# Kernel tuning notes

Hardware: AMD Instinct MI355X
Metric: run time of the kernel (lower is better)

Reference implementation:

```python
import jax, jax.numpy as jnp
import numpy as np

T, H = 2048, 1024          # tokens, hidden_size
NH, NKV, D = 16, 4, 64     # heads, kv heads, head_dim
E, F = 8, 1024             # experts, intermediate_size
TOPK = 1
EPS = 1e-5
THETA = 500000.0
SCALE = D ** -0.5


def rmsnorm(x, w=None, eps=EPS):
    # fp32 accumulation like vLLM RMSNorm
    v = jnp.mean(x.astype(jnp.float32) ** 2, axis=-1, keepdims=True)
    y = x.astype(jnp.float32) * jax.lax.rsqrt(v + eps)
    y = y.astype(x.dtype)
    return y * w if w is not None else y


def setup_inputs() -> dict:
    key = jax.random.key(0)
    ks = jax.random.split(key, 12)
    s = 1.0 / np.sqrt(H)
    sf = 1.0 / np.sqrt(F)
    return {
        "positions": jnp.arange(T, dtype=jnp.int32),
        "hidden_states": jax.random.normal(ks[0], (T, H), jnp.float32),
        "ln1_w": jnp.ones((H,), jnp.float32),
        "ln2_w": jnp.ones((H,), jnp.float32),
        "wqkv": jax.random.normal(ks[1], (H, (NH + 2 * NKV) * D), jnp.float32) * s,
        "wo": jax.random.normal(ks[2], (NH * D, H), jnp.float32) * s,
        "router_w": jax.random.normal(ks[3], (H, E), jnp.float32) * s,
        "w_gate": jax.random.normal(ks[4], (E, H, F), jnp.float32) * s,
        "w_up": jax.random.normal(ks[5], (E, H, F), jnp.float32) * s,
        "w_down": jax.random.normal(ks[6], (E, F, H), jnp.float32) * sf,
        "sh_gate": jax.random.normal(ks[7], (H, F), jnp.float32) * s,
        "sh_up": jax.random.normal(ks[8], (H, F), jnp.float32) * s,
        "sh_down": jax.random.normal(ks[9], (F, H), jnp.float32) * sf,
    }


def reference(positions, hidden_states, ln1_w, ln2_w, wqkv, wo, router_w,
              w_gate, w_up, w_down, sh_gate, sh_up, sh_down):
    # --- input_layernorm (residual is None on first call) ---
    residual = hidden_states
    h = rmsnorm(hidden_states, ln1_w)

    # --- attention: qkv proj ---
    qkv = h @ wqkv
    q = qkv[:, : NH * D].reshape(T, NH, D)
    k = qkv[:, NH * D: (NH + NKV) * D].reshape(T, NKV, D)
    v = qkv[:, (NH + NKV) * D:].reshape(T, NKV, D)

    # --- neox-style RoPE ---
    half = D // 2
    inv_freq = 1.0 / (THETA ** (jnp.arange(half, dtype=jnp.float32) / half))
    ang = positions.astype(jnp.float32)[:, None] * inv_freq[None, :]
    cos = jnp.cos(ang)[:, None, :]  # [T,1,half]
    sin = jnp.sin(ang)[:, None, :]

    def rope(x):
        x1, x2 = x[..., :half], x[..., half:]
        return jnp.concatenate([x1 * cos - x2 * sin, x2 * cos + x1 * sin], axis=-1)

    q = rope(q)
    k = rope(k)

    # --- fp32 QK-RMSNorm (no weight), applied after RoPE as in source ---
    q = rmsnorm(q)
    k = rmsnorm(k)

    # --- GQA causal attention ---
    n_rep = NH // NKV
    kr = jnp.repeat(k, n_rep, axis=1)  # [T,NH,D]
    vr = jnp.repeat(v, n_rep, axis=1)
    scores = jnp.einsum('thd,shd->hts', q, kr) * SCALE  # [NH,T,T]
    causal = positions[:, None] >= positions[None, :]
    scores = jnp.where(causal[None], scores, -jnp.inf)
    attn = jax.nn.softmax(scores, axis=-1)
    ao = jnp.einsum('hts,shd->thd', attn, vr).reshape(T, NH * D)
    h = ao @ wo

    # --- post_attention_layernorm with fused residual add ---
    x = h + residual
    residual = x
    h = rmsnorm(x, ln2_w)

    # --- MoE: top-1 sigmoid router, router weight applied on input ---
    logits = h @ router_w                      # [T,E]
    score, idx = jax.lax.top_k(logits, TOPK)   # [T,1]
    gate = jax.nn.sigmoid(score.astype(jnp.float32)).astype(h.dtype)
    x_in = h * gate                            # apply_router_weight_on_input
    onehot = (idx == jnp.arange(E)[None, :]).astype(h.dtype)  # [T,E]
    g = jax.nn.silu(jnp.einsum('th,ehf->tef', x_in, w_gate)) \
        * jnp.einsum('th,ehf->tef', x_in, w_up)               # [T,E,F]
    out_e = jnp.einsum('tef,efh->teh', g, w_down)             # [T,E,H]
    routed = jnp.einsum('teh,te->th', out_e, onehot)

    # --- shared expert (SiLU MLP) ---
    shared = (jax.nn.silu(h @ sh_gate) * (h @ sh_up)) @ sh_down

    out = routed + shared
    return (out, residual)
```

## Files before the change

### kernel.cpp

```cpp
#include <hip/hip_runtime.h>
#include <hip/hip_bf16.h>
#include <cmath>
#include <cstdint>

#define T 2048
#define H 1024
#define NH 16
#define NKV 4
#define DH 64
#define NE 8
#define FF 1024
#define QKVN ((NH + 2 * NKV) * DH)
#define EPS 1e-5f
#define ATTN_SCALE 0.125f
#define LOG2E 1.44269504f
#define MBOUND 12.0f
#define ASPLIT 4

typedef short bf16x8 __attribute__((ext_vector_type(8)));
typedef float floatx4 __attribute__((ext_vector_type(4)));

__device__ __forceinline__ void gload16(const void* g, void* l) {
  __builtin_amdgcn_global_load_lds((const __attribute__((address_space(1))) void*)g,
                                   (__attribute__((address_space(3))) void*)l, 16, 0, 0);
}

__global__ __launch_bounds__(256) void rmsnorm1024(const float* __restrict__ x,
                                                   const float* __restrict__ w,
                                                   __hip_bfloat16* __restrict__ yb) {
  int row = blockIdx.x;
  const float4* x4 = (const float4*)(x + (size_t)row * H);
  float4 v = x4[threadIdx.x];
  float s = v.x * v.x + v.y * v.y + v.z * v.z + v.w * v.w;
  #pragma unroll
  for (int o = 32; o; o >>= 1) s += __shfl_down(s, o, 64);
  __shared__ float red[4];
  if ((threadIdx.x & 63) == 0) red[threadIdx.x >> 6] = s;
  __syncthreads();
  s = red[0] + red[1] + red[2] + red[3];
  float inv = rsqrtf(s * (1.0f / (float)H) + EPS);
  float4 wv = ((const float4*)w)[threadIdx.x];
  __hip_bfloat16* yp = yb + (size_t)row * H + threadIdx.x * 4;
  yp[0] = __float2bfloat16(v.x * inv * wv.x);
  yp[1] = __float2bfloat16(v.y * inv * wv.y);
  yp[2] = __float2bfloat16(v.z * inv * wv.z);
  yp[3] = __float2bfloat16(v.w * inv * wv.w);
}

__global__ __launch_bounds__(256) void fused_add_rms(const float* __restrict__ a,
                                                     const float* __restrict__ b,
                                                     float* __restrict__ resid,
                                                     const float* __restrict__ w,
                                                     float* __restrict__ yf,
                                                     __hip_bfloat16* __restrict__ yb,
                                                     int* __restrict__ counts_g) {
  int row = blockIdx.x;
  if (row == 0 && threadIdx.x < 2 * NE) counts_g[threadIdx.x] = 0;
  float4 av = ((const float4*)(a + (size_t)row * H))[threadIdx.x];
  float4 bv = ((const float4*)(b + (size_t)row * H))[threadIdx.x];
  float4 v = make_float4(av.x + bv.x, av.y + bv.y, av.z + bv.z, av.w + bv.w);
  ((float4*)(resid + (size_t)row * H))[threadIdx.x] = v;
  float s = v.x * v.x + v.y * v.y + v.z * v.z + v.w * v.w;
  #pragma unroll
  for (int o = 32; o; o >>= 1) s += __shfl_down(s, o, 64);
  __shared__ float red[4];
  if ((threadIdx.x & 63) == 0) red[threadIdx.x >> 6] = s;
  __syncthreads();
  s = red[0] + red[1] + red[2] + red[3];
  float inv = rsqrtf(s * (1.0f / (float)H) + EPS);
  float4 wv = ((const float4*)w)[threadIdx.x];
  float o0 = v.x * inv * wv.x, o1 = v.y * inv * wv.y, o2 = v.z * inv * wv.z, o3 = v.w * inv * wv.w;
  ((float4*)(yf + (size_t)row * H))[threadIdx.x] = make_float4(o0, o1, o2, o3);
  __hip_bfloat16* yp = yb + (size_t)row * H + threadIdx.x * 4;
  yp[0] = __float2bfloat16(o0);
  yp[1] = __float2bfloat16(o1);
  yp[2] = __float2bfloat16(o2);
  yp[3] = __float2bfloat16(o3);
}

__global__ __launch_bounds__(256) void tcast9(const float* __restrict__ srcE,
                                              const float* __restrict__ srcS,
                                              __hip_bfloat16* __restrict__ dst, int R, int C,
                                              long long srcStride, long long dstStride,
                                              long long sBatch, long long dBatch) {
  int z = blockIdx.z;
  const float* src = (srcS && z == (int)gridDim.z - 1) ? srcS : srcE + (long long)z * sBatch;
  dst += (long long)z * dBatch;
  int c0 = blockIdx.x * 64, r0 = blockIdx.y * 32;
  __shared__ float tile[32][65];
  int tid = threadIdx.x;
  int lr = tid >> 4;
  int lc = (tid & 15) * 4;
  #pragma unroll
  for (int it = 0; it < 2; it++) {
    float4 v = *(const float4*)(src + (long long)(r0 + lr + it * 16) * srcStride + c0 + lc);
    tile[lr + it * 16][lc + 0] = v.x;
    tile[lr + it * 16][lc + 1] = v.y;
    tile[lr + it * 16][lc + 2] = v.z;
    tile[lr + it * 16][lc + 3] = v.w;
  }
  __syncthreads();
  int oc = tid >> 2;
  int rr = (tid & 3) * 8;
  short ov[8];
  #pragma unroll
  for (int i = 0; i < 8; i++) {
    __hip_bfloat16 b = __float2bfloat16(tile[rr + i][oc]);
    ov[i] = *(short*)&b;
  }
  *(bf16x8*)((short*)dst + (long long)(c0 + oc) * dstStride + r0 + rr) = *(bf16x8*)ov;
}

__global__ __launch_bounds__(256) void gemm_bf16(const __hip_bfloat16* __restrict__ A,
                                                 const __hip_bfloat16* __restrict__ A2,
                                                 const __hip_bfloat16* __restrict__ Bt,
                                                 void* __restrict__ Cout, void* __restrict__ Cout2,
                                                 int M, int N, int K, int out_bf16,
                                                 const int* __restrict__ row_offs,
                                                 long long strideB,
                                                 const int* __restrict__ permA,
                                                 const float* __restrict__ gatev) {
  int e = blockIdx.z;
  bool sh = (A2 != nullptr && e == (int)gridDim.z - 1);
  int rbeg = 0, rend = M;
  const __hip_bfloat16* Ap = A;
  void* Cp = Cout;
  const int* pA = permA;
  if (sh) {
    Ap = A2; Cp = Cout2; pA = nullptr;
  } else if (row_offs) {
    rbeg = row_offs[e]; rend = row_offs[e + 1];
  }
  long long m0 = rbeg + (long long)blockIdx.y * 128;
  if (m0 >= rend) return;
  long long n0 = (long long)blockIdx.x * 64;
  const __hip_bfloat16* Bp = Bt + (long long)e * strideB;

  __shared__ unsigned short As[2][128 * 64];
  __shared__ unsigned short Bs[2][64 * 64];

  int tid = threadIdx.x;
  int lane = tid & 63, w = tid >> 6;
  int wr = (w >> 1) * 64, wc = (w & 1) * 32;
  int qd = lane >> 4, ln16 = lane & 15;
  int l7 = ln16 & 7;

  floatx4 acc[4][2];
  floatx4 zero = {0.f, 0.f, 0.f, 0.f};
  #pragma unroll
  for (int i = 0; i < 4; i++)
    #pragma unroll
    for (int j = 0; j < 2; j++) acc[i][j] = zero;

  int rowA[4], kcA[4];
  const unsigned short* Arow[4];
  const unsigned short* Brow[2];
  #pragma unroll
  for (int it = 0; it < 4; it++) {
    int chunk = tid + it * 256;
    rowA[it] = chunk >> 3;
    kcA[it] = ((chunk & 7) ^ (rowA[it] & 7)) * 8;
    long long ra = m0 + rowA[it];
    if (ra >= rend) ra = rend - 1;
    long long tok = pA ? (long long)pA[ra] : ra;
    Arow[it] = (const unsigned short*)Ap + tok * K;
  }
  #pragma unroll
  for (int it = 0; it < 2; it++)
    Brow[it] = (const unsigned short*)Bp + (n0 + rowA[it]) * K;

  #pragma unroll
  for (int it = 0; it < 4; it++)
    gload16(Arow[it] + kcA[it], As[0] + (tid + it * 256) * 8);
  #pragma unroll
  for (int it = 0; it < 2; it++)
    gload16(Brow[it] + kcA[it], Bs[0] + (tid + it * 256) * 8);
  __syncthreads();

  int cur = 0;
  for (int k0 = 0; k0 < K; k0 += 64) {
    int kn = k0 + 64;
    if (kn < K) {
      #pragma unroll
      for (int it = 0; it < 4; it++)
        gload16(Arow[it] + kn + kcA[it], As[cur ^ 1] + (tid + it * 256) * 8);
      #pragma unroll
      for (int it = 0; it < 2; it++)
        gload16(Brow[it] + kn + kcA[it], Bs[cur ^ 1] + (tid + it * 256) * 8);
    }
    const unsigned short* Ac = As[cur];
    const unsigned short* Bc = Bs[cur];
    #pragma unroll
    for (int s = 0; s < 2; s++) {
      bf16x8 af[4], bfr[2];
      #pragma unroll
      for (int i = 0; i < 4; i++) {
        int row = wr + i * 16 + ln16;
        af[i] = *(const bf16x8*)(Ac + row * 64 + (((s * 4 + qd) ^ l7) * 8));
      }
      #pragma unroll
      for (int j = 0; j < 2; j++) {
        int row = wc + j * 16 + ln16;
        bfr[j] = *(const bf16x8*)(Bc + row * 64 + (((s * 4 + qd) ^ l7) * 8));
      }
      #pragma unroll
      for (int i = 0; i < 4; i++)
        #pragma unroll
        for (int j = 0; j < 2; j++)
          acc[i][j] = __builtin_amdgcn_mfma_f32_16x16x32_bf16(af[i], bfr[j], acc[i][j], 0, 0, 0);
    }
    __syncthreads();
    cur ^= 1;
  }

  #pragma unroll
  for (int i = 0; i < 4; i++) {
    #pragma unroll
    for (int r = 0; r < 4; r++) {
      long long gm = m0 + wr + i * 16 + qd * 4 + r;
      if (gm < rend) {
        float gsc = 1.0f;
        if (pA && gatev) gsc = gatev[pA[gm]];
        #pragma unroll
        for (int j = 0; j < 2; j++) {
          long long gn = n0 + wc + j * 16 + ln16;
          float v = acc[i][j][r] * gsc;
          if (out_bf16)
            ((__hip_bfloat16*)Cp)[gm * N + gn] = __float2bfloat16(v);
          else
            ((float*)Cp)[gm * N + gn] = v;
        }
      }
    }
  }
}

__global__ __launch_bounds__(256) void rope_pack(const float* __restrict__ qkv,
                                                 const int* __restrict__ positions,
                                                 __hip_bfloat16* __restrict__ Qb,
                                                 __hip_bfloat16* __restrict__ Kb) {
  int b = blockIdx.x * 4 + (threadIdx.x >> 6);
  int t = b / (NH + NKV);
  int hh = b % (NH + NKV);
  const float* ptr = qkv + (long long)t * QKVN + hh * DH;
  int d = threadIdx.x & 63;
  float v = ptr[d];
  int fi = d & 31;
  float inv_freq = exp2f(-(float)fi * (18.93156857f / 32.0f));
  float ang = (float)positions[t] * inv_freq;
  float c = __cosf(ang), s = __sinf(ang);
  float other = __shfl_xor(v, 32, 64);
  float r = (d < 32) ? (v * c - other * s) : (v * c + other * s);
  float sq = r * r;
  #pragma unroll
  for (int off = 32; off; off >>= 1) sq += __shfl_xor(sq, off, 64);
  float o = r * rsqrtf(sq * (1.0f / (float)DH) + EPS);
  if (hh < NH)
    Qb[(size_t)t * (NH * DH) + hh * DH + d] = __float2bfloat16(o * (ATTN_SCALE * LOG2E));
  else
    Kb[(size_t)t * (NKV * DH) + (hh - NH) * DH + d] = __float2bfloat16(o);
}

__global__ __launch_bounds__(256, 2) void attn_mfma(const __hip_bfloat16* __restrict__ Qb,
                                                    const __hip_bfloat16* __restrict__ Kbuf,
                                                    const __hip_bfloat16* __restrict__ VtG,
                                                    float* __restrict__ Opart,
                                                    float* __restrict__ Lpart) {
  int kvh = blockIdx.y;
  int qi = blockIdx.x;
  int sp = blockIdx.z;
  int q0 = qi * 64;
  int nt = qi + 1;
  if (sp >= nt) return;

  __shared__ unsigned short Ks[2][64 * 64];
  __shared__ unsigned short Vs[2][64 * 64];
  __shared__ unsigned short Ps[4 * 16 * 64];

  int tid = threadIdx.x;
  int lane = tid & 63, w = tid >> 6;
  int h = kvh * 4 + w;
  int qd = lane >> 4, ln16 = lane & 15;
  int l7 = ln16 & 7;
  unsigned short* Pw = Ps + w * 16 * 64;

  int r0 = tid >> 3;
  int sc = ((tid & 7) ^ (r0 & 7)) * 8;

  const unsigned short* KbP = (const unsigned short*)Kbuf;
  const unsigned short* VtP = (const unsigned short*)VtG;

  bf16x8 aq[4][2];
  #pragma unroll
  for (int rt = 0; rt < 4; rt++) {
    const unsigned short* qp =
        (const unsigned short*)Qb + (size_t)(q0 + rt * 16 + ln16) * (NH * DH) + h * DH;
    aq[rt][0] = *(const bf16x8*)(qp + qd * 8);
    aq[rt][1] = *(const bf16x8*)(qp + 32 + qd * 8);
  }

  bf16x8 ones;
  #pragma unroll
  for (int i = 0; i < 8; i++) ones[i] = (short)0x3F80;

  floatx4 O_[4][4], accl[4];
  floatx4 zero = {0.f, 0.f, 0.f, 0.f};
  #pragma unroll
  for (int rt = 0; rt < 4; rt++) {
    #pragma unroll
    for (int j = 0; j < 4; j++) O_[rt][j] = zero;
    accl[rt] = zero;
  }

  {
    int kb = sp * 64;
    gload16(KbP + (size_t)(kb + r0) * (NKV * DH) + kvh * DH + sc, Ks[0] + tid * 8);
    gload16(KbP + (size_t)(kb + r0 + 32) * (NKV * DH) + kvh * DH + sc, Ks[0] + tid * 8 + 2048);
    gload16(VtP + (size_t)(kvh * DH + r0) * T + kb + sc, Vs[0] + tid * 8);
    gload16(VtP + (size_t)(kvh * DH + r0 + 32) * T + kb + sc, Vs[0] + tid * 8 + 2048);
  }
  __syncthreads();

  int cur = 0;
  for (int kt = sp; kt < nt; kt += ASPLIT) {
    int ktn = kt + ASPLIT;
    if (ktn < nt) {
      int kb = ktn * 64;
      unsigned short* Kn = Ks[cur ^ 1];
      unsigned short* Vn = Vs[cur ^ 1];
      gload16(KbP + (size_t)(kb + r0) * (NKV * DH) + kvh * DH + sc, Kn + tid * 8);
      gload16(KbP + (size_t)(kb + r0 + 32) * (NKV * DH) + kvh * DH + sc, Kn + tid * 8 + 2048);
      gload16(VtP + (size_t)(kvh * DH + r0) * T + kb + sc, Vn + tid * 8);
      gload16(VtP + (size_t)(kvh * DH + r0 + 32) * T + kb + sc, Vn + tid * 8 + 2048);
    }
    const unsigned short* Kc = Ks[cur];
    const unsigned short* Vc = Vs[cur];
    int kb = kt * 64;

    #pragma unroll
    for (int rt = 0; rt < 4; rt++) {
      floatx4 S_[4];
      #pragma unroll
      for (int j = 0; j < 4; j++) S_[j] = zero;
      #pragma unroll
      for (int s = 0; s < 2; s++) {
        bf16x8 bk[4];
        #pragma unroll
        for (int j = 0; j < 4; j++)
          bk[j] = *(const bf16x8*)(Kc + (j * 16 + ln16) * 64 + (((s * 4 + qd) ^ l7) * 8));
        #pragma unroll
        for (int j = 0; j < 4; j++)
          S_[j] = __builtin_amdgcn_mfma_f32_16x16x32_bf16(aq[rt][s], bk[j], S_[j], 0, 0, 0);
      }

      int tq_base = q0 + rt * 16 + qd * 4;
      if (kb + 63 > q0 + rt * 16) {
        #pragma unroll
        for (int j = 0; j < 4; j++) {
          int tk = kb + j * 16 + ln16;
          #pragma unroll
          for (int r = 0; r < 4; r++)
            S_[j][r] = (tk <= tq_base + r) ? exp2f(S_[j][r] - MBOUND) : 0.f;
        }
      } else {
        #pragma unroll
        for (int j = 0; j < 4; j++)
          #pragma unroll
          for (int r = 0; r < 4; r++) S_[j][r] = exp2f(S_[j][r] - MBOUND);
      }

      #pragma unroll
      for (int j = 0; j < 4; j++)
        #pragma unroll
        for (int r = 0; r < 4; r++) {
          int row = qd * 4 + r;
          int pc = (((j * 2 + (ln16 >> 3)) ^ (row & 7)) * 8) + l7;
          __hip_bfloat16 pb = __float2bfloat16(S_[j][r]);
          Pw[row * 64 + pc] = *(unsigned short*)&pb;
        }

      #pragma unroll
      for (int s = 0; s < 2; s++) {
        bf16x8 ap = *(const bf16x8*)(Pw + ln16 * 64 + (((s * 4 + qd) ^ l7) * 8));
        bf16x8 bv[4];
        #pragma unroll
        for (int j = 0; j < 4; j++)
          bv[j] = *(const bf16x8*)(Vc + (j * 16 + ln16) * 64 + (((s * 4 + qd) ^ l7) * 8));
        #pragma unroll
        for (int j = 0; j < 4; j++)
          O_[rt][j] = __builtin_amdgcn_mfma_f32_16x16x32_bf16(ap, bv[j], O_[rt][j], 0, 0, 0);
        accl[rt] = __builtin_amdgcn_mfma_f32_16x16x32_bf16(ap, ones, accl[rt], 0, 0, 0);
      }
    }
    __syncthreads();
    cur ^= 1;
  }

  size_t pbase = ((size_t)(qi * NH + h) * ASPLIT + sp) * (64 * 64);
  #pragma unroll
  for (int rt = 0; rt < 4; rt++) {
    int rl_base = rt * 16 + qd * 4;
    #pragma unroll
    for (int j = 0; j < 4; j++)
      #pragma unroll
      for (int r = 0; r < 4; r++)
        Opart[pbase + (size_t)(rl_base + r) * 64 + j * 16 + ln16] = O_[rt][j][r];
  }
  if (ln16 == 0) {
    size_t lbase = ((size_t)(qi * NH + h) * ASPLIT + sp) * 64;
    #pragma unroll
    for (int rt = 0; rt < 4; rt++)
      #pragma unroll
      for (int r = 0; r < 4; r++) Lpart[lbase + rt * 16 + qd * 4 + r] = accl[rt][r];
  }
}

__global__ __launch_bounds__(256) void attn_combine(const float* __restrict__ Opart,
                                                    const float* __restrict__ Lpart,
                                                    __hip_bfloat16* __restrict__ ao) {
  int qi = blockIdx.x, h = blockIdx.y;
  int nv = (qi + 1 < ASPLIT) ? (qi + 1) : ASPLIT;
  int row = threadIdx.x >> 2;
  int c0 = (threadIdx.x & 3) * 16;
  size_t base = (size_t)(qi * NH + h) * ASPLIT * 4096;
  size_t lb = (size_t)(qi * NH + h) * ASPLIT * 64;
  float l = 0.f;
  float acc[16];
  #pragma unroll
  for (int i = 0; i < 16; i++) acc[i] = 0.f;
  for (int s = 0; s < nv; s++) {
    const float* Op = Opart + base + (size_t)s * 4096 + (size_t)row * 64 + c0;
    l += Lpart[lb + s * 64 + row];
    #pragma unroll
    for (int i = 0; i < 16; i += 4) {
      float4 v = *(const float4*)(Op + i);
      acc[i] += v.x; acc[i + 1] += v.y; acc[i + 2] += v.z; acc[i + 3] += v.w;
    }
  }
  float inv = 1.f / l;
  int t = qi * 64 + row;
  short ov[16];
  #pragma unroll
  for (int i = 0; i < 16; i++) {
    __hip_bfloat16 b = __float2bfloat16(acc[i] * inv);
    ov[i] = *(short*)&b;
  }
  short* dst = (short*)ao + (size_t)t * (NH * DH) + h * DH + c0;
  *(bf16x8*)dst = *(bf16x8*)&ov[0];
  *(bf16x8*)(dst + 8) = *(bf16x8*)&ov[8];
}

__global__ __launch_bounds__(256) void silumul_both(const __hip_bfloat16* __restrict__ gA2,
                                                    const __hip_bfloat16* __restrict__ gS2,
                                                    __hip_bfloat16* __restrict__ gP,
                                                    __hip_bfloat16* __restrict__ gPs,
                                                    int n8each) {
  int i = blockIdx.x * blockDim.x + threadIdx.x;
  const __hip_bfloat16* src = gA2;
  __hip_bfloat16* dst = gP;
  if (i >= n8each) {
    i -= n8each;
    src = gS2;
    dst = gPs;
  }
  int el = i * 8;
  int row = el >> 10;
  int c = el & (FF - 1);
  const unsigned short* g = (const unsigned short*)src + (size_t)row * (2 * FF) + c;
  bf16x8 a8 = *(const bf16x8*)g;
  bf16x8 b8 = *(const bf16x8*)(g + FF);
  short o8[8];
  #pragma unroll
  for (int k = 0; k < 8; k++) {
    short sa = a8[k], sb = b8[k];
    float av = __bfloat162float(*(__hip_bfloat16*)&sa);
    float bv = __bfloat162float(*(__hip_bfloat16*)&sb);
    __hip_bfloat16 ob = __float2bfloat16(av / (1.f + __expf(-av)) * bv);
    o8[k] = *(short*)&ob;
  }
  *(bf16x8*)((unsigned short*)dst + el) = *(bf16x8*)o8;
}

__global__ __launch_bounds__(64) void router_kernel(const float* __restrict__ h2,
                                                    const float* __restrict__ rw,
                                                    int* __restrict__ idx,
                                                    float* __restrict__ gate,
                                                    int* __restrict__ counts) {
  int t = blockIdx.x;
  int lane = threadIdx.x;
  float acc[NE] = {};
  for (int k = lane; k < H; k += 64) {
    float hv = h2[(long long)t * H + k];
    float4 r0 = *(const float4*)(rw + (long long)k * NE);
    float4 r1 = *(const float4*)(rw + (long long)k * NE + 4);
    acc[0] += hv * r0.x; acc[1] += hv * r0.y; acc[2] += hv * r0.z; acc[3] += hv * r0.w;
    acc[4] += hv * r1.x; acc[5] += hv * r1.y; acc[6] += hv * r1.z; acc[7] += hv * r1.w;
  }
  #pragma unroll
  for (int off = 32; off; off >>= 1)
    #pragma unroll
    for (int e2 = 0; e2 < NE; e2++) acc[e2] += __shfl_down(acc[e2], off, 64);
  if (lane == 0) {
    int best = 0;
    float bv = acc[0];
    #pragma unroll
    for (int e2 = 1; e2 < NE; e2++)
      if (acc[e2] > bv) { bv = acc[e2]; best = e2; }
    idx[t] = best;
    gate[t] = 1.f / (1.f + expf(-bv));
    atomicAdd(&counts[best], 1);
  }
}

__global__ __launch_bounds__(256) void assign_scan(const int* __restrict__ counts,
                                                   const int* __restrict__ idx,
                                                   int* __restrict__ offs,
                                                   int* __restrict__ cnt2,
                                                   int* __restrict__ perm,
                                                   int* __restrict__ pos) {
  __shared__ int offs_s[NE + 1];
  if (threadIdx.x == 0) {
    int s = 0;
    for (int e2 = 0; e2 < NE; e2++) { offs_s[e2] = s; offs[e2] = s; s += counts[e2]; }
    offs_s[NE] = s; offs[NE] = s;
  }
  __syncthreads();
  for (int t = threadIdx.x; t < T; t += 256) {
    int e2 = idx[t];
    int p = offs_s[e2] + atomicAdd(&cnt2[e2], 1);
    pos[t] = p;
    perm[p] = t;
  }
}

__global__ __launch_bounds__(256) void final_add_kernel(float* __restrict__ out,
                                                        const float* __restrict__ outp,
                                                        const int* __restrict__ pos) {
  int t = blockIdx.x;
  int p = pos[t];
  const float4* src = (const float4*)(outp + (long long)p * H);
  float4* dst = (float4*)(out + (long long)t * H);
  float4 a = dst[threadIdx.x];
  float4 b = src[threadIdx.x];
  a.x += b.x; a.y += b.y; a.z += b.z; a.w += b.w;
  dst[threadIdx.x] = a;
}

extern "C" void kernel_launch(void* const* d_in, const int* in_sizes, int n_in,
                              void* d_out, int out_size, void* d_ws, size_t ws_size,
                              hipStream_t stream) {
  const int* positions = (const int*)d_in[0];
  const float* hidden = (const float*)d_in[1];
  const float* ln1_w = (const float*)d_in[2];
  const float* ln2_w = (const float*)d_in[3];
  const float* wqkv = (const float*)d_in[4];
  const float* wo = (const float*)d_in[5];
  const float* router_w = (const float*)d_in[6];
  const float* w_gate = (const float*)d_in[7];
  const float* w_up = (const float*)d_in[8];
  const float* w_down = (const float*)d_in[9];
  const float* sh_gate = (const float*)d_in[10];
  const float* sh_up = (const float*)d_in[11];
  const float* sh_down = (const float*)d_in[12];

  float* out = (float*)d_out;
  float* resid = out + (size_t)T * H;

  char* p = (char*)d_ws;
  auto alloc = [&](size_t bytes) { char* r = p; p += (bytes + 255) & ~(size_t)255; return r; };

  float* qkv = (float*)alloc((size_t)T * QKVN * 4);
  float* h2 = (float*)alloc((size_t)T * H * 4);
  float* gb1 = (float*)alloc((size_t)T * H * 4);
  float* outp = (float*)alloc((size_t)T * H * 4);
  __hip_bfloat16* h1b = (__hip_bfloat16*)alloc((size_t)T * H * 2);
  __hip_bfloat16* aob = (__hip_bfloat16*)alloc((size_t)T * H * 2);
  __hip_bfloat16* h2b = (__hip_bfloat16*)alloc((size_t)T * H * 2);
  __hip_bfloat16* gA2 = (__hip_bfloat16*)alloc((size_t)T * 2 * FF * 2);
  __hip_bfloat16* gP = (__hip_bfloat16*)alloc((size_t)T * FF * 2);
  __hip_bfloat16* Qb = (__hip_bfloat16*)alloc((size_t)T * NH * DH * 2);
  __hip_bfloat16* Kb = (__hip_bfloat16*)alloc((size_t)T * NKV * DH * 2);
  __hip_bfloat16* VtG = (__hip_bfloat16*)alloc((size_t)NKV * DH * T * 2);
  __hip_bfloat16* wqkvT = (__hip_bfloat16*)alloc((size_t)H * QKVN * 2);
  __hip_bfloat16* woT = (__hip_bfloat16*)alloc((size_t)H * H * 2);
  __hip_bfloat16* wguT = (__hip_bfloat16*)alloc((size_t)9 * 2 * FF * H * 2);
  __hip_bfloat16* wdT = (__hip_bfloat16*)alloc((size_t)9 * H * FF * 2);
  int* counts = (int*)alloc(2 * NE * 4);
  int* cnt2 = counts + NE;
  int* offs = (int*)alloc((NE + 1) * 4);
  int* idx = (int*)alloc(T * 4);
  int* perm = (int*)alloc(T * 4);
  int* pos = (int*)alloc(T * 4);
  float* gate = (float*)alloc(T * 4);

  __hip_bfloat16* gS2 = (__hip_bfloat16*)gb1;
  __hip_bfloat16* gPs = h1b;

  float* Opart = qkv;
  float* Lpart = qkv + (size_t)(T / 64) * NH * ASPLIT * 4096;

  tcast9<<<dim3(QKVN / 64, H / 32, 1), 256, 0, stream>>>(wqkv, nullptr, wqkvT, H, QKVN, QKVN, H, 0, 0);
  tcast9<<<dim3(H / 64, H / 32, 1), 256, 0, stream>>>(wo, nullptr, woT, H, H, H, H, 0, 0);
  tcast9<<<dim3(FF / 64, H / 32, 9), 256, 0, stream>>>(w_gate, sh_gate, wguT, H, FF, FF, H,
                                                       (long long)H * FF, (long long)2 * H * FF);
  tcast9<<<dim3(FF / 64, H / 32, 9), 256, 0, stream>>>(w_up, sh_up, wguT + (size_t)FF * H, H, FF, FF, H,
                                                       (long long)H * FF, (long long)2 * H * FF);
  tcast9<<<dim3(H / 64, FF / 32, 9), 256, 0, stream>>>(w_down, sh_down, wdT, FF, H, H, FF,
                                                       (long long)FF * H, (long long)H * FF);

  rmsnorm1024<<<T, 256, 0, stream>>>(hidden, ln1_w, h1b);
  gemm_bf16<<<dim3(QKVN / 64, T / 128, 1), 256, 0, stream>>>(h1b, nullptr, wqkvT, qkv, nullptr,
                                                             T, QKVN, H, 0, nullptr, 0, nullptr, nullptr);
  rope_pack<<<T * (NH + NKV) / 4, 256, 0, stream>>>(qkv, positions, Qb, Kb);
  tcast9<<<dim3(NKV * DH / 64, T / 32, 1), 256, 0, stream>>>(qkv + (NH + NKV) * DH, nullptr, VtG,
                                                             T, NKV * DH, QKVN, T, 0, 0);
  attn_mfma<<<dim3(T / 64, NKV, ASPLIT), 256, 0, stream>>>(Qb, Kb, VtG, Opart, Lpart);
  attn_combine<<<dim3(T / 64, NH), 256, 0, stream>>>(Opart, Lpart, aob);
  gemm_bf16<<<dim3(H / 64, T / 128, 1), 256, 0, stream>>>(aob, nullptr, woT, gb1, nullptr,
                                                          T, H, H, 0, nullptr, 0, nullptr, nullptr);
  fused_add_rms<<<T, 256, 0, stream>>>(gb1, hidden, resid, ln2_w, h2, h2b, counts);
  router_kernel<<<T, 64, 0, stream>>>(h2, router_w, idx, gate, counts);
  assign_scan<<<1, 256, 0, stream>>>(counts, idx, offs, cnt2, perm, pos);
  gemm_bf16<<<dim3(2 * FF / 64, T / 128, 9), 256, 0, stream>>>(h2b, h2b, wguT, gA2, gS2,
                                                               T, 2 * FF, H, 1, offs,
                                                               (long long)2 * H * FF, perm, gate);
  silumul_both<<<(2 * T * FF / 8) / 256, 256, 0, stream>>>(gA2, gS2, gP, gPs, T * FF / 8);
  gemm_bf16<<<dim3(H / 64, T / 128, 9), 256, 0, stream>>>(gP, gPs, wdT, outp, out,
                                                          T, H, FF, 0, offs, (long long)FF * H,
                                                          nullptr, nullptr);
  final_add_kernel<<<T, 256, 0, stream>>>(out, outp, pos);
}
```

Baseline: 394.9 us.

## Fuse RoPE/QK-norm/V-transpose into QKV GEMM epilogue and residual add into O-proj

Adds a dedicated QKV GEMM whose 64-wide column tiles align with heads, so the epilogue applies RoPE, per-head RMS normalisation and scaling directly and writes bf16 Q/K, or transposes V through LDS into VtG. This removes the fp32 qkv round trip plus the separate rope_pack and transpose launches. The output-projection GEMM now adds the residual in its epilogue, reducing fused_add_rms to a plain RMS norm. The trade-off is a heavier GEMM epilogue with per-element sincos and more register pressure.

```diff
diff --git a/kernel.cpp b/kernel.cpp
--- a/kernel.cpp
+++ b/kernel.cpp
@@ -47,19 +47,14 @@
   yp[3] = __float2bfloat16(v.w * inv * wv.w);
 }
 
-__global__ __launch_bounds__(256) void fused_add_rms(const float* __restrict__ a,
-                                                     const float* __restrict__ b,
-                                                     float* __restrict__ resid,
-                                                     const float* __restrict__ w,
-                                                     float* __restrict__ yf,
-                                                     __hip_bfloat16* __restrict__ yb,
-                                                     int* __restrict__ counts_g) {
+__global__ __launch_bounds__(256) void rms_h2(const float* __restrict__ x,
+                                              const float* __restrict__ w,
+                                              float* __restrict__ yf,
+                                              __hip_bfloat16* __restrict__ yb,
+                                              int* __restrict__ counts_g) {
   int row = blockIdx.x;
   if (row == 0 && threadIdx.x < 2 * NE) counts_g[threadIdx.x] = 0;
-  float4 av = ((const float4*)(a + (size_t)row * H))[threadIdx.x];
-  float4 bv = ((const float4*)(b + (size_t)row * H))[threadIdx.x];
-  float4 v = make_float4(av.x + bv.x, av.y + bv.y, av.z + bv.z, av.w + bv.w);
-  ((float4*)(resid + (size_t)row * H))[threadIdx.x] = v;
+  float4 v = ((const float4*)(x + (size_t)row * H))[threadIdx.x];
   float s = v.x * v.x + v.y * v.y + v.z * v.z + v.w * v.w;
   #pragma unroll
   for (int o = 32; o; o >>= 1) s += __shfl_down(s, o, 64);
@@ -119,7 +114,8 @@
                                                  const int* __restrict__ row_offs,
                                                  long long strideB,
                                                  const int* __restrict__ permA,
-                                                 const float* __restrict__ gatev) {
+                                                 const float* __restrict__ gatev,
+                                                 const float* __restrict__ addC) {
   int e = blockIdx.z;
   bool sh = (A2 != nullptr && e == (int)gridDim.z - 1);
   int rbeg = 0, rend = M;
@@ -225,6 +221,7 @@
         for (int j = 0; j < 2; j++) {
           long long gn = n0 + wc + j * 16 + ln16;
           float v = acc[i][j][r] * gsc;
+          if (addC) v += addC[gm * N + gn];
           if (out_bf16)
             ((__hip_bfloat16*)Cp)[gm * N + gn] = __float2bfloat16(v);
           else
@@ -235,30 +232,146 @@
   }
 }
 
-__global__ __launch_bounds__(256) void rope_pack(const float* __restrict__ qkv,
-                                                 const int* __restrict__ positions,
-                                                 __hip_bfloat16* __restrict__ Qb,
-                                                 __hip_bfloat16* __restrict__ Kb) {
-  int b = blockIdx.x * 4 + (threadIdx.x >> 6);
-  int t = b / (NH + NKV);
-  int hh = b % (NH + NKV);
-  const float* ptr = qkv + (long long)t * QKVN + hh * DH;
-  int d = threadIdx.x & 63;
-  float v = ptr[d];
-  int fi = d & 31;
-  float inv_freq = exp2f(-(float)fi * (18.93156857f / 32.0f));
-  float ang = (float)positions[t] * inv_freq;
-  float c = __cosf(ang), s = __sinf(ang);
-  float other = __shfl_xor(v, 32, 64);
-  float r = (d < 32) ? (v * c - other * s) : (v * c + other * s);
-  float sq = r * r;
-  #pragma unroll
-  for (int off = 32; off; off >>= 1) sq += __shfl_xor(sq, off, 64);
-  float o = r * rsqrtf(sq * (1.0f / (float)DH) + EPS);
-  if (hh < NH)
-    Qb[(size_t)t * (NH * DH) + hh * DH + d] = __float2bfloat16(o * (ATTN_SCALE * LOG2E));
-  else
-    Kb[(size_t)t * (NKV * DH) + (hh - NH) * DH + d] = __float2bfloat16(o);
+__global__ __launch_bounds__(256) void gemm_qkv(const __hip_bfloat16* __restrict__ A,
+                                                const __hip_bfloat16* __restrict__ Bt,
+                                                const int* __restrict__ positions,
+                                                __hip_bfloat16* __restrict__ Qb,
+                                                __hip_bfloat16* __restrict__ Kb,
+                                                __hip_bfloat16* __restrict__ VtG) {
+  const int K = H;
+  long long m0 = (long long)blockIdx.y * 128;
+  long long n0 = (long long)blockIdx.x * 64;
+
+  __shared__ unsigned short As[2][128 * 64];
+  __shared__ unsigned short Bs[2][64 * 64];
+
+  int tid = threadIdx.x;
+  int lane = tid & 63, w = tid >> 6;
+  int qd = lane >> 4, ln16 = lane & 15;
+  int l7 = ln16 & 7;
+
+  floatx4 acc[2][4];
+  floatx4 zero = {0.f, 0.f, 0.f, 0.f};
+  #pragma unroll
+  for (int i = 0; i < 2; i++)
+    #pragma unroll
+    for (int j = 0; j < 4; j++) acc[i][j] = zero;
+
+  int rowA[4], kcA[4];
+  const unsigned short* Arow[4];
+  const unsigned short* Brow[2];
+  #pragma unroll
+  for (int it = 0; it < 4; it++) {
+    int chunk = tid + it * 256;
+    rowA[it] = chunk >> 3;
+    kcA[it] = ((chunk & 7) ^ (rowA[it] & 7)) * 8;
+    Arow[it] = (const unsigned short*)A + (m0 + rowA[it]) * K;
+  }
+  #pragma unroll
+  for (int it = 0; it < 2; it++)
+    Brow[it] = (const unsigned short*)Bt + (n0 + rowA[it]) * K;
+
+  #pragma unroll
+  for (int it = 0; it < 4; it++)
+    gload16(Arow[it] + kcA[it], As[0] + (tid + it * 256) * 8);
+  #pragma unroll
+  for (int it = 0; it < 2; it++)
+    gload16(Brow[it] + kcA[it], Bs[0] + (tid + it * 256) * 8);
+  __syncthreads();
+
+  int cur = 0;
+  for (int k0 = 0; k0 < K; k0 += 64) {
+    int kn = k0 + 64;
+    if (kn < K) {
+      #pragma unroll
+      for (int it = 0; it < 4; it++)
+        gload16(Arow[it] + kn + kcA[it], As[cur ^ 1] + (tid + it * 256) * 8);
+      #pragma unroll
+      for (int it = 0; it < 2; it++)
+        gload16(Brow[it] + kn + kcA[it], Bs[cur ^ 1] + (tid + it * 256) * 8);
+    }
+    const unsigned short* Ac = As[cur];
+    const unsigned short* Bc = Bs[cur];
+    #pragma unroll
+    for (int s = 0; s < 2; s++) {
+      bf16x8 af[2], bfr[4];
+      #pragma unroll
+      for (int i = 0; i < 2; i++) {
+        int row = w * 32 + i * 16 + ln16;
+        af[i] = *(const bf16x8*)(Ac + row * 64 + (((s * 4 + qd) ^ l7) * 8));
+      }
+      #pragma unroll
+      for (int j = 0; j < 4; j++) {
+        int row = j * 16 + ln16;
+        bfr[j] = *(const bf16x8*)(Bc + row * 64 + (((s * 4 + qd) ^ l7) * 8));
+      }
+      #pragma unroll
+      for (int i = 0; i < 2; i++)
+        #pragma unroll
+        for (int j = 0; j < 4; j++)
+          acc[i][j] = __builtin_amdgcn_mfma_f32_16x16x32_bf16(af[i], bfr[j], acc[i][j], 0, 0, 0);
+    }
+    __syncthreads();
+    cur ^= 1;
+  }
+
+  int hh = blockIdx.x;
+  if (hh < NH + NKV) {
+    bool isq = hh < NH;
+    float invf0 = exp2f(-(float)ln16 * (18.93156857f / 32.0f));
+    float invf1 = exp2f(-(float)(ln16 + 16) * (18.93156857f / 32.0f));
+    #pragma unroll
+    for (int i = 0; i < 2; i++) {
+      #pragma unroll
+      for (int r = 0; r < 4; r++) {
+        int t = (int)m0 + w * 32 + i * 16 + qd * 4 + r;
+        float pos = (float)positions[t];
+        float c0, s0, c1, s1;
+        __sincosf(pos * invf0, &s0, &c0);
+        __sincosf(pos * invf1, &s1, &c1);
+        float v0 = acc[i][0][r], v1 = acc[i][1][r], v2 = acc[i][2][r], v3 = acc[i][3][r];
+        float ro0 = v0 * c0 - v2 * s0;
+        float ro1 = v1 * c1 - v3 * s1;
+        float ro2 = v2 * c0 + v0 * s0;
+        float ro3 = v3 * c1 + v1 * s1;
+        float sq = ro0 * ro0 + ro1 * ro1 + ro2 * ro2 + ro3 * ro3;
+        sq += __shfl_xor(sq, 1, 64);
+        sq += __shfl_xor(sq, 2, 64);
+        sq += __shfl_xor(sq, 4, 64);
+        sq += __shfl_xor(sq, 8, 64);
+        float inv = rsqrtf(sq * (1.0f / (float)DH) + EPS);
+        if (isq) inv *= (ATTN_SCALE * LOG2E);
+        __hip_bfloat16* dst = isq ? (Qb + (size_t)t * (NH * DH) + hh * DH)
+                                  : (Kb + (size_t)t * (NKV * DH) + (hh - NH) * DH);
+        dst[0 * 16 + ln16] = __float2bfloat16(ro0 * inv);
+        dst[1 * 16 + ln16] = __float2bfloat16(ro1 * inv);
+        dst[2 * 16 + ln16] = __float2bfloat16(ro2 * inv);
+        dst[3 * 16 + ln16] = __float2bfloat16(ro3 * inv);
+      }
+    }
+  } else {
+    unsigned short* sw = ((unsigned short*)As) + w * 2560;
+    #pragma unroll
+    for (int i = 0; i < 2; i++)
+      #pragma unroll
+      for (int j = 0; j < 4; j++)
+        #pragma unroll
+        for (int r = 0; r < 4; r++) {
+          __hip_bfloat16 b = __float2bfloat16(acc[i][j][r]);
+          sw[(j * 16 + ln16) * 40 + i * 16 + qd * 4 + r] = *(unsigned short*)&b;
+        }
+    int d = lane;
+    int t0 = (int)m0 + w * 32;
+    const unsigned short* sr = sw + d * 40;
+    unsigned short* vd = (unsigned short*)VtG + (size_t)((hh - NH - NKV) * DH + d) * T + t0;
+    #pragma unroll
+    for (int kk = 0; kk < 4; kk++) {
+      short tmp[8];
+      #pragma unroll
+      for (int q2 = 0; q2 < 8; q2++) tmp[q2] = sr[kk * 8 + q2];
+      *(bf16x8*)(vd + kk * 8) = *(bf16x8*)tmp;
+    }
+  }
 }
 
 __global__ __launch_bounds__(256, 2) void attn_mfma(const __hip_bfloat16* __restrict__ Qb,
@@ -609,24 +722,22 @@
                                                        (long long)FF * H, (long long)H * FF);
 
   rmsnorm1024<<<T, 256, 0, stream>>>(hidden, ln1_w, h1b);
-  gemm_bf16<<<dim3(QKVN / 64, T / 128, 1), 256, 0, stream>>>(h1b, nullptr, wqkvT, qkv, nullptr,
-                                                             T, QKVN, H, 0, nullptr, 0, nullptr, nullptr);
-  rope_pack<<<T * (NH + NKV) / 4, 256, 0, stream>>>(qkv, positions, Qb, Kb);
-  tcast9<<<dim3(NKV * DH / 64, T / 32, 1), 256, 0, stream>>>(qkv + (NH + NKV) * DH, nullptr, VtG,
-                                                             T, NKV * DH, QKVN, T, 0, 0);
+  gemm_qkv<<<dim3(QKVN / 64, T / 128), 256, 0, stream>>>(h1b, wqkvT, positions, Qb, Kb, VtG);
   attn_mfma<<<dim3(T / 64, NKV, ASPLIT), 256, 0, stream>>>(Qb, Kb, VtG, Opart, Lpart);
   attn_combine<<<dim3(T / 64, NH), 256, 0, stream>>>(Opart, Lpart, aob);
-  gemm_bf16<<<dim3(H / 64, T / 128, 1), 256, 0, stream>>>(aob, nullptr, woT, gb1, nullptr,
-                                                          T, H, H, 0, nullptr, 0, nullptr, nullptr);
-  fused_add_rms<<<T, 256, 0, stream>>>(gb1, hidden, resid, ln2_w, h2, h2b, counts);
+  gemm_bf16<<<dim3(H / 64, T / 128, 1), 256, 0, stream>>>(aob, nullptr, woT, resid, nullptr,
+                                                          T, H, H, 0, nullptr, 0, nullptr, nullptr,
+                                                          hidden);
+  rms_h2<<<T, 256, 0, stream>>>(resid, ln2_w, h2, h2b, counts);
   router_kernel<<<T, 64, 0, stream>>>(h2, router_w, idx, gate, counts);
   assign_scan<<<1, 256, 0, stream>>>(counts, idx, offs, cnt2, perm, pos);
   gemm_bf16<<<dim3(2 * FF / 64, T / 128, 9), 256, 0, stream>>>(h2b, h2b, wguT, gA2, gS2,
                                                                T, 2 * FF, H, 1, offs,
-                                                               (long long)2 * H * FF, perm, gate);
+                                                               (long long)2 * H * FF, perm, gate,
+                                                               nullptr);
   silumul_both<<<(2 * T * FF / 8) / 256, 256, 0, stream>>>(gA2, gS2, gP, gPs, T * FF / 8);
   gemm_bf16<<<dim3(H / 64, T / 128, 9), 256, 0, stream>>>(gP, gPs, wdT, outp, out,
                                                           T, H, FF, 0, offs, (long long)FF * H,
-                                                          nullptr, nullptr);
+                                                          nullptr, nullptr, nullptr);
   final_add_kernel<<<T, 256, 0, stream>>>(out, outp, pos);
 }
```

New measurement: 394.0 us. Within noise of the previous version (-0.2%).
